# Performance work log

Measured on AMD Instinct MI355X. Metric: run time of the kernel, lower is better.

## Reference

```python
import jax, jax.numpy as jnp
import numpy as np

N_NODES = 100000
DROP_P = 0.1


def gcn_conv(x, W, b, row, col, n_nodes):
    """PyG GCNConv: out = D^{-1/2}(A+I)D^{-1/2} X W + b.
    row/col already include self-loops. Messages flow row(src) -> col(dst)."""
    xw = x @ W  # [N, H]
    deg = jax.ops.segment_sum(jnp.ones_like(col, dtype=xw.dtype), col, num_segments=n_nodes)
    dinv = jnp.where(deg > 0, jax.lax.rsqrt(deg), 0.0)
    norm = dinv[row] * dinv[col]  # [E]
    msg = norm[:, None] * xw[row]  # [E, H] gather + scale
    out = jax.ops.segment_sum(msg, col, num_segments=n_nodes)  # scatter-add
    return out + b


def dropout(x, key, p):
    keep = jax.random.bernoulli(key, 1.0 - p, x.shape)
    return jnp.where(keep, x / (1.0 - p), 0.0).astype(x.dtype)


def prelu(x, alpha):
    return jnp.where(x >= 0, x, alpha[None, :] * x)


def setup_inputs() -> dict:
    key = jax.random.key(0)
    k1, k2, k3, k4 = jax.random.split(key, 4)
    in_ch, hid = 128, 128
    n_edges = 1600000
    x = jax.random.normal(k1, (N_NODES, in_ch), dtype=jnp.float32)
    edge_index = jax.random.randint(k2, (2, n_edges), 0, N_NODES, dtype=jnp.int64)
    s = 1.0 / np.sqrt(in_ch)
    W1 = jax.random.normal(k3, (in_ch, hid), dtype=jnp.float32) * s
    W2 = jax.random.normal(k4, (hid, hid), dtype=jnp.float32) * s
    b1 = jnp.zeros((hid,), dtype=jnp.float32)
    b2 = jnp.zeros((hid,), dtype=jnp.float32)
    alpha = jnp.full((hid,), 0.25, dtype=jnp.float32)
    return {"x": x, "edge_index": edge_index, "W1": W1, "b1": b1,
            "W2": W2, "b2": b2, "alpha": alpha}


def reference(x, edge_index, W1, b1, W2, b2, alpha):
    n = x.shape[0]
    # add self-loops once (PyG default add_self_loops=True)
    loop = jnp.arange(n, dtype=edge_index.dtype)
    row = jnp.concatenate([edge_index[0], loop])
    col = jnp.concatenate([edge_index[1], loop])

    dk1, dk2 = jax.random.split(jax.random.key(42))
    h = gcn_conv(x, W1, b1, row, col, n)
    h = dropout(h, dk1, DROP_P)
    h = prelu(h, alpha)
    h = gcn_conv(h, W2, b2, row, col, n)
    h = dropout(h, dk2, DROP_P)
    h = prelu(h, alpha)
    return h
```

## Files before the change

### kernel.cpp

```cpp
#include <hip/hip_runtime.h>
#include <stdint.h>
#include <string.h>

__host__ __device__ inline uint32_t rotl32(uint32_t x, int r) {
    return (x << r) | (x >> (32 - r));
}

__host__ __device__ inline void tf2x32(uint32_t k0, uint32_t k1,
                                       uint32_t x0, uint32_t x1,
                                       uint32_t& o0, uint32_t& o1) {
    uint32_t ks0 = k0, ks1 = k1, ks2 = k0 ^ k1 ^ 0x1BD11BDAu;
    x0 += ks0; x1 += ks1;
#define TF_R4(a,b,c,d) \
    x0 += x1; x1 = rotl32(x1,a); x1 ^= x0; \
    x0 += x1; x1 = rotl32(x1,b); x1 ^= x0; \
    x0 += x1; x1 = rotl32(x1,c); x1 ^= x0; \
    x0 += x1; x1 = rotl32(x1,d); x1 ^= x0;
    TF_R4(13,15,26,6)  x0 += ks1; x1 += ks2 + 1u;
    TF_R4(17,29,16,24) x0 += ks2; x1 += ks0 + 2u;
    TF_R4(13,15,26,6)  x0 += ks0; x1 += ks1 + 3u;
    TF_R4(17,29,16,24) x0 += ks1; x1 += ks2 + 4u;
    TF_R4(13,15,26,6)  x0 += ks2; x1 += ks0 + 5u;
#undef TF_R4
    o0 = x0; o1 = x1;
}

__device__ inline unsigned pk2h(float a, float b) {
    _Float16 ha = (_Float16)a, hb = (_Float16)b;
    unsigned short ua, ub;
    __builtin_memcpy(&ua, &ha, 2);
    __builtin_memcpy(&ub, &hb, 2);
    return (unsigned)ua | ((unsigned)ub << 16);
}
__device__ inline unsigned short h16bits(float a) {
    _Float16 h = (_Float16)a;
    unsigned short u; __builtin_memcpy(&u, &h, 2);
    return u;
}
__device__ inline float lo16(unsigned u) {
    unsigned short s = (unsigned short)(u & 0xffffu);
    _Float16 h; __builtin_memcpy(&h, &s, 2);
    return (float)h;
}
__device__ inline float hi16(unsigned u) {
    unsigned short s = (unsigned short)(u >> 16);
    _Float16 h; __builtin_memcpy(&h, &s, 2);
    return (float)h;
}

typedef float fx4 __attribute__((ext_vector_type(4)));
typedef unsigned ux4 __attribute__((ext_vector_type(4)));
typedef _Float16 h16x8 __attribute__((ext_vector_type(8)));
typedef _Float16 h16x2 __attribute__((ext_vector_type(2)));
typedef float f32x4 __attribute__((ext_vector_type(4)));

__device__ inline h16x2 as_h2(unsigned u) { h16x2 r; __builtin_memcpy(&r, &u, 4); return r; }

#define CSR_CAP 48
#define NBKT 256
#define PART_EPB 8192

__global__ __launch_bounds__(256) void k_part(
        const int* __restrict__ ei, long long* __restrict__ gbkt,
        unsigned* __restrict__ gbcnt, int E, int N, int bw, int bcap) {
    __shared__ unsigned hcnt[NBKT], hoff[NBKT], hrun[NBKT];
    int t = (int)threadIdx.x;
    int base = blockIdx.x * PART_EPB;
    hcnt[t] = 0; hrun[t] = 0;
    __syncthreads();
    for (int i = 0; i < PART_EPB / 256; ++i) {
        int e = base + i * 256 + t;
        if (e < E) {
            int c = __builtin_nontemporal_load(ei + (size_t)E + e);
            int r = __builtin_nontemporal_load(ei + e);
            if ((unsigned)c < (unsigned)N && (unsigned)r < (unsigned)N)
                atomicAdd(&hcnt[(unsigned)c / (unsigned)bw], 1u);
        }
    }
    __syncthreads();
    hoff[t] = atomicAdd(&gbcnt[t], hcnt[t]);
    __syncthreads();
    for (int i = 0; i < PART_EPB / 256; ++i) {
        int e = base + i * 256 + t;
        if (e < E) {
            int c = ei[(size_t)E + e];
            int r = ei[e];
            if ((unsigned)c < (unsigned)N && (unsigned)r < (unsigned)N) {
                unsigned sp = (unsigned)c / (unsigned)bw;
                unsigned rank = atomicAdd(&hrun[sp], 1u);
                unsigned gp = hoff[sp] + rank;
                if (gp < (unsigned)bcap)
                    gbkt[(size_t)sp * bcap + gp] =
                        (long long)(unsigned)r | ((long long)(unsigned)c << 32);
            }
        }
    }
}

__global__ __launch_bounds__(256) void k_work(
        const long long* __restrict__ gbkt, const unsigned* __restrict__ gbcnt,
        unsigned* __restrict__ cnt, unsigned* __restrict__ csr,
        unsigned long long* __restrict__ m1, unsigned long long* __restrict__ m2,
        const float* __restrict__ x, unsigned* __restrict__ xb,
        const float* __restrict__ w1, const float* __restrict__ w2,
        _Float16* __restrict__ wt1, _Float16* __restrict__ wt2,
        unsigned k1a, unsigned k1b, unsigned k2a, unsigned k2b,
        int N, int bw, int bcap, int total, int MB, int CB) {
    __shared__ unsigned lcnt[512];
    int b = blockIdx.x;
    int t = (int)threadIdx.x;
    if (b < NBKT) {
        int lo = b * bw;
        int hi = lo + bw; if (hi > N) hi = N;
        int w = hi - lo; if (w < 0) w = 0;
        lcnt[t] = 0; lcnt[t + 256] = 0;
        __syncthreads();
        unsigned ne = gbcnt[b];
        if (ne > (unsigned)bcap) ne = (unsigned)bcap;
        const long long* base = gbkt + (size_t)b * bcap;
        for (unsigned e = t; e < ne; e += 256) {
            long long v = __builtin_nontemporal_load(base + e);
            unsigned r = (unsigned)(v & 0xffffffffll);
            unsigned c = (unsigned)(v >> 32);
            unsigned slot = atomicAdd(&lcnt[c - (unsigned)lo], 1u);
            if (slot < (unsigned)CSR_CAP)
                csr[(size_t)c * CSR_CAP + slot] = r;
        }
        __syncthreads();
        for (int i = t; i < w; i += 256)
            cnt[lo + i] = lcnt[i];
        return;
    }
    b -= NBKT;
    if (b < MB) {
        int wv = (b * 256 + t) >> 6;
        int lane = t & 63;
        int TW = (2 * total) >> 6;
        int half = total >> 6;
        int w0 = wv * 8;
#pragma unroll
        for (int j = 0; j < 8; j++) {
            int wd = w0 + j;
            if (wd < TW) {
                int wl = wd;
                unsigned ka = k1a, kb = k1b;
                unsigned long long* m = m1;
                if (wl >= half) { wl -= half; ka = k2a; kb = k2b; m = m2; }
                uint32_t o0, o1;
                tf2x32(ka, kb, 0u, (uint32_t)(wl * 64 + lane), o0, o1);
                bool keep = (((o0 ^ o1) >> 9) < 7549747u);
                unsigned long long bal = __ballot(keep);
                if (lane == 0)
                    __builtin_nontemporal_store(bal, m + wl);
            }
        }
        return;
    }
    b -= MB;
    if (b < CB) {
        int i = b * 256 + t;
        if (i < (total >> 3)) {
            const fx4* src = (const fx4*)(x + (size_t)i * 8);
            fx4 a = __builtin_nontemporal_load(src);
            fx4 bb = __builtin_nontemporal_load(src + 1);
            ux4 v;
            v.x = pk2h(a.x, a.y);
            v.y = pk2h(a.z, a.w);
            v.z = pk2h(bb.x, bb.y);
            v.w = pk2h(bb.z, bb.w);
            __builtin_nontemporal_store(v, (ux4*)xb + i);
        }
        return;
    }
    b -= CB;
    int idx = b * 256 + t;
    int mat = idx >> 14;
    int e2 = idx & 16383;
    int c = e2 >> 7, k = e2 & 127;
    const float* W = mat ? w2 : w1;
    _Float16* WT = mat ? wt2 : wt1;
    WT[(size_t)c * 128 + k] = (_Float16)W[(size_t)k * 128 + c];
}

__global__ __launch_bounds__(256) void k_prep(const unsigned* __restrict__ cnt,
        float* __restrict__ dinv, uint4* __restrict__ xb4, int N) {
    int i = blockIdx.x * 256 + (int)threadIdx.x;
    int node = i >> 4, part = i & 15;
    if (node >= N) return;
    float d = rsqrtf((float)cnt[node] + 1.0f);
    if (part == 0) dinv[node] = d;
    uint4 u = xb4[(size_t)node * 16 + part];
    uint4 o;
    o.x = pk2h(d * lo16(u.x), d * hi16(u.x));
    o.y = pk2h(d * lo16(u.y), d * hi16(u.y));
    o.z = pk2h(d * lo16(u.z), d * hi16(u.z));
    o.w = pk2h(d * lo16(u.w), d * hi16(u.w));
    xb4[(size_t)node * 16 + part] = o;
}

template <int OUT_HALF>
__global__ __launch_bounds__(128, 8) void k_layer(
        const unsigned short* __restrict__ in,
        const _Float16* __restrict__ WT,
        const float* __restrict__ bias, const float* __restrict__ alpha,
        const unsigned long long* __restrict__ mask,
        const float* __restrict__ dinv, const unsigned* __restrict__ cnt,
        const unsigned* __restrict__ csr,
        void* outv, int n) {
    __shared__ unsigned hls[32 * 68];
    int t = (int)threadIdx.x;
    int wv = t >> 6;
    int l = t & 63;
    int rowbase = blockIdx.x * 32 + wv * 16;
    unsigned* hl = hls + wv * 16 * 68;
    int slot = l >> 4;
    int lm = l & 15;
    int ci = lm << 3;

    int prow = rowbase + lm;
    bool pv = prow < n;
    float dnAll = pv ? dinv[prow] : 0.f;
    unsigned cAll = pv ? cnt[prow] : 0u;
    if (cAll > (unsigned)CSR_CAP) cAll = (unsigned)CSR_CAP;

#pragma unroll
    for (int g = 0; g < 4; ++g) {
        int rloc = g * 4 + slot;
        int node = rowbase + rloc;
        float dn = __shfl(dnAll, rloc);
        unsigned ecnt = (unsigned)__shfl((int)cAll, rloc);
        h16x2 a0 = (h16x2)0, a1 = (h16x2)0, a2 = (h16x2)0, a3 = (h16x2)0;
        size_t eb = (size_t)node * CSR_CAP;
        unsigned e = 0;
        unsigned nb4 = ecnt >> 2;
#pragma unroll 2
        for (unsigned bb = 0; bb < nb4; ++bb) {
            ux4 rr = __builtin_nontemporal_load((const ux4*)(csr + eb + e));
            uint4 u0 = *(const uint4*)(in + ((size_t)rr.x << 7) + ci);
            uint4 u1 = *(const uint4*)(in + ((size_t)rr.y << 7) + ci);
            uint4 u2 = *(const uint4*)(in + ((size_t)rr.z << 7) + ci);
            uint4 u3 = *(const uint4*)(in + ((size_t)rr.w << 7) + ci);
            a0 += as_h2(u0.x); a1 += as_h2(u0.y); a2 += as_h2(u0.z); a3 += as_h2(u0.w);
            a0 += as_h2(u1.x); a1 += as_h2(u1.y); a2 += as_h2(u1.z); a3 += as_h2(u1.w);
            a0 += as_h2(u2.x); a1 += as_h2(u2.y); a2 += as_h2(u2.z); a3 += as_h2(u2.w);
            a0 += as_h2(u3.x); a1 += as_h2(u3.y); a2 += as_h2(u3.z); a3 += as_h2(u3.w);
            e += 4;
        }
        for (; e < ecnt; ++e) {
            unsigned r0 = csr[eb + e];
            uint4 u0 = *(const uint4*)(in + ((size_t)r0 << 7) + ci);
            a0 += as_h2(u0.x); a1 += as_h2(u0.y); a2 += as_h2(u0.z); a3 += as_h2(u0.w);
        }
        if (node < n) {
            uint4 sv = *(const uint4*)(in + ((size_t)node << 7) + ci);
            a0 += as_h2(sv.x); a1 += as_h2(sv.y); a2 += as_h2(sv.z); a3 += as_h2(sv.w);
        }
        uint4 o;
        o.x = pk2h(dn * (float)a0[0], dn * (float)a0[1]);
        o.y = pk2h(dn * (float)a1[0], dn * (float)a1[1]);
        o.z = pk2h(dn * (float)a2[0], dn * (float)a2[1]);
        o.w = pk2h(dn * (float)a3[0], dn * (float)a3[1]);
        *(uint4*)(hl + (size_t)rloc * 68 + lm * 4) = o;
    }

    int kq = l >> 4;
    h16x8 afr[4];
#pragma unroll
    for (int kk = 0; kk < 4; kk++)
        afr[kk] = *(const h16x8*)(hl + (size_t)lm * 68 + kq * 4 + kk * 16);
#pragma unroll
    for (int f = 0; f < 8; f++) {
        f32x4 acc = (f32x4){0.f, 0.f, 0.f, 0.f};
#pragma unroll
        for (int kk = 0; kk < 4; kk++) {
            h16x8 bfr = *(const h16x8*)(WT + (size_t)(f * 16 + lm) * 128 + kk * 32 + kq * 8);
            acc = __builtin_amdgcn_mfma_f32_16x16x32_f16(afr[kk], bfr, acc, 0, 0, 0);
        }
        int c = f * 16 + lm;
        float bs = bias[c];
        float al = alpha[c];
#pragma unroll
        for (int j = 0; j < 4; j++) {
            int rl = kq * 4 + j;
            int rg = rowbase + rl;
            if (rg < n) {
                unsigned long long wmw = mask[((size_t)rg << 1) + (f >> 2)];
                bool keep = (wmw >> (c & 63)) & 1ull;
                float v = acc[j] + bs;
                v = keep ? v * (1.0f / 0.9f) : 0.0f;
                v = (v >= 0.f) ? v : al * v;
                if (OUT_HALF) {
                    float dnrow = __shfl(dnAll, rl);
                    __builtin_nontemporal_store(h16bits(v * dnrow),
                        (unsigned short*)outv + (size_t)rg * 128 + c);
                } else {
                    __builtin_nontemporal_store(v,
                        (float*)outv + (size_t)rg * 128 + c);
                }
            }
        }
    }
}

extern "C" void kernel_launch(void* const* d_in, const int* in_sizes, int n_in,
                              void* d_out, int out_size, void* d_ws, size_t ws_size,
                              hipStream_t stream) {
    const float* x  = (const float*)d_in[0];
    const int*   ei = (const int*)d_in[1];
    const float* W1 = (const float*)d_in[2];
    const float* b1 = (const float*)d_in[3];
    const float* W2 = (const float*)d_in[4];
    const float* b2 = (const float*)d_in[5];
    const float* al = (const float*)d_in[6];
    int N = in_sizes[0] / 128;
    int E = in_sizes[1] / 2;
    float* out = (float*)d_out;

    int bw = (N + NBKT - 1) / NBKT;
    int bcap = E / NBKT + E / NBKT / 4 + 1024;

    char* p = (char*)d_ws;
    unsigned short* xb = (unsigned short*)p;   p += (size_t)N * 128 * 2;
    unsigned short* ab = (unsigned short*)p;   p += (size_t)N * 128 * 2;
    long long* gbkt = (long long*)ab;
    unsigned* cnt = (unsigned*)p;              p += (size_t)N * 4;
    float* dinv = (float*)p;                   p += (size_t)N * 4;
    unsigned* csr = (unsigned*)p;              p += (size_t)N * CSR_CAP * 4;
    unsigned long long* m1 = (unsigned long long*)p;  p += ((size_t)N * 128 / 64) * 8;
    unsigned long long* m2 = (unsigned long long*)p;  p += ((size_t)N * 128 / 64) * 8;
    _Float16* wt1 = (_Float16*)p;              p += 128 * 128 * 2;
    _Float16* wt2 = (_Float16*)p;              p += 128 * 128 * 2;
    unsigned* gbcnt = (unsigned*)p;

    hipMemsetAsync(gbcnt, 0, NBKT * 4, stream);

    uint32_t dk1a, dk1b, dk2a, dk2b;
    tf2x32(0u, 42u, 0u, 0u, dk1a, dk1b);
    tf2x32(0u, 42u, 0u, 1u, dk2a, dk2b);

    int total = N * 128;
    int P1A = (E + PART_EPB - 1) / PART_EPB;
    k_part<<<P1A, 256, 0, stream>>>(ei, gbkt, gbcnt, E, N, bw, bcap);

    int TW = (2 * total) / 64;
    int MB = (TW + 31) / 32;
    int CB = (total / 8 + 255) / 256;
    int WB = (2 * 128 * 128 + 255) / 256;
    k_work<<<NBKT + MB + CB + WB, 256, 0, stream>>>(gbkt, gbcnt, cnt, csr,
                                                    m1, m2, x, (unsigned*)xb,
                                                    W1, W2, wt1, wt2,
                                                    dk1a, dk1b, dk2a, dk2b,
                                                    N, bw, bcap, total, MB, CB);
    k_prep<<<(N * 16 + 255) / 256, 256, 0, stream>>>(cnt, dinv, (uint4*)xb, N);

    int LB = (N + 31) / 32;
    k_layer<1><<<LB, 128, 0, stream>>>(xb, wt1, b1, al, m1, dinv, cnt, csr, ab, N);
    k_layer<0><<<LB, 128, 0, stream>>>(ab, wt2, b2, al, m2, dinv, cnt, csr, out, N);
}
```

Measured before the change: 322.2 us.

## Regroup preprocessing kernels: merge partition with mask/convert, fuse CSR build with scaling

The edge partition pass now runs in the same launch as dropout-mask generation, x conversion and weight transpose. The CSR-bucket build is fused with the dinv computation and the degree scaling of x, so the separate k_prep launch goes away. This cuts one kernel launch and lets the independent partition and elementwise work overlap. In exchange, the CSR/scale kernel now runs on only 256 blocks, so the scaling pass has less parallelism per node range.

```diff
diff --git a/kernel.cpp b/kernel.cpp
--- a/kernel.cpp
+++ b/kernel.cpp
@@ -62,76 +62,51 @@
 
 __global__ __launch_bounds__(256) void k_part(
         const int* __restrict__ ei, long long* __restrict__ gbkt,
-        unsigned* __restrict__ gbcnt, int E, int N, int bw, int bcap) {
-    __shared__ unsigned hcnt[NBKT], hoff[NBKT], hrun[NBKT];
-    int t = (int)threadIdx.x;
-    int base = blockIdx.x * PART_EPB;
-    hcnt[t] = 0; hrun[t] = 0;
-    __syncthreads();
-    for (int i = 0; i < PART_EPB / 256; ++i) {
-        int e = base + i * 256 + t;
-        if (e < E) {
-            int c = __builtin_nontemporal_load(ei + (size_t)E + e);
-            int r = __builtin_nontemporal_load(ei + e);
-            if ((unsigned)c < (unsigned)N && (unsigned)r < (unsigned)N)
-                atomicAdd(&hcnt[(unsigned)c / (unsigned)bw], 1u);
-        }
-    }
-    __syncthreads();
-    hoff[t] = atomicAdd(&gbcnt[t], hcnt[t]);
-    __syncthreads();
-    for (int i = 0; i < PART_EPB / 256; ++i) {
-        int e = base + i * 256 + t;
-        if (e < E) {
-            int c = ei[(size_t)E + e];
-            int r = ei[e];
-            if ((unsigned)c < (unsigned)N && (unsigned)r < (unsigned)N) {
-                unsigned sp = (unsigned)c / (unsigned)bw;
-                unsigned rank = atomicAdd(&hrun[sp], 1u);
-                unsigned gp = hoff[sp] + rank;
-                if (gp < (unsigned)bcap)
-                    gbkt[(size_t)sp * bcap + gp] =
-                        (long long)(unsigned)r | ((long long)(unsigned)c << 32);
-            }
-        }
-    }
-}
-
-__global__ __launch_bounds__(256) void k_work(
-        const long long* __restrict__ gbkt, const unsigned* __restrict__ gbcnt,
-        unsigned* __restrict__ cnt, unsigned* __restrict__ csr,
+        unsigned* __restrict__ gbcnt,
         unsigned long long* __restrict__ m1, unsigned long long* __restrict__ m2,
         const float* __restrict__ x, unsigned* __restrict__ xb,
         const float* __restrict__ w1, const float* __restrict__ w2,
         _Float16* __restrict__ wt1, _Float16* __restrict__ wt2,
         unsigned k1a, unsigned k1b, unsigned k2a, unsigned k2b,
-        int N, int bw, int bcap, int total, int MB, int CB) {
-    __shared__ unsigned lcnt[512];
+        int E, int N, int bw, int bcap, int total,
+        int PB, int MB, int CB) {
+    __shared__ unsigned hcnt[NBKT], hoff[NBKT], hrun[NBKT];
     int b = blockIdx.x;
     int t = (int)threadIdx.x;
-    if (b < NBKT) {
-        int lo = b * bw;
-        int hi = lo + bw; if (hi > N) hi = N;
-        int w = hi - lo; if (w < 0) w = 0;
-        lcnt[t] = 0; lcnt[t + 256] = 0;
+    if (b < PB) {
+        int base = b * PART_EPB;
+        hcnt[t] = 0; hrun[t] = 0;
         __syncthreads();
-        unsigned ne = gbcnt[b];
-        if (ne > (unsigned)bcap) ne = (unsigned)bcap;
-        const long long* base = gbkt + (size_t)b * bcap;
-        for (unsigned e = t; e < ne; e += 256) {
-            long long v = __builtin_nontemporal_load(base + e);
-            unsigned r = (unsigned)(v & 0xffffffffll);
-            unsigned c = (unsigned)(v >> 32);
-            unsigned slot = atomicAdd(&lcnt[c - (unsigned)lo], 1u);
-            if (slot < (unsigned)CSR_CAP)
-                csr[(size_t)c * CSR_CAP + slot] = r;
+        for (int i = 0; i < PART_EPB / 256; ++i) {
+            int e = base + i * 256 + t;
+            if (e < E) {
+                int c = __builtin_nontemporal_load(ei + (size_t)E + e);
+                int r = __builtin_nontemporal_load(ei + e);
+                if ((unsigned)c < (unsigned)N && (unsigned)r < (unsigned)N)
+                    atomicAdd(&hcnt[(unsigned)c / (unsigned)bw], 1u);
+            }
         }
         __syncthreads();
-        for (int i = t; i < w; i += 256)
-            cnt[lo + i] = lcnt[i];
+        hoff[t] = atomicAdd(&gbcnt[t], hcnt[t]);
+        __syncthreads();
+        for (int i = 0; i < PART_EPB / 256; ++i) {
+            int e = base + i * 256 + t;
+            if (e < E) {
+                int c = ei[(size_t)E + e];
+                int r = ei[e];
+                if ((unsigned)c < (unsigned)N && (unsigned)r < (unsigned)N) {
+                    unsigned sp = (unsigned)c / (unsigned)bw;
+                    unsigned rank = atomicAdd(&hrun[sp], 1u);
+                    unsigned gp = hoff[sp] + rank;
+                    if (gp < (unsigned)bcap)
+                        gbkt[(size_t)sp * bcap + gp] =
+                            (long long)(unsigned)r | ((long long)(unsigned)c << 32);
+                }
+            }
+        }
         return;
     }
-    b -= NBKT;
+    b -= PB;
     if (b < MB) {
         int wv = (b * 256 + t) >> 6;
         int lane = t & 63;
@@ -182,20 +157,46 @@
     WT[(size_t)c * 128 + k] = (_Float16)W[(size_t)k * 128 + c];
 }
 
-__global__ __launch_bounds__(256) void k_prep(const unsigned* __restrict__ cnt,
-        float* __restrict__ dinv, uint4* __restrict__ xb4, int N) {
-    int i = blockIdx.x * 256 + (int)threadIdx.x;
-    int node = i >> 4, part = i & 15;
-    if (node >= N) return;
-    float d = rsqrtf((float)cnt[node] + 1.0f);
-    if (part == 0) dinv[node] = d;
-    uint4 u = xb4[(size_t)node * 16 + part];
-    uint4 o;
-    o.x = pk2h(d * lo16(u.x), d * hi16(u.x));
-    o.y = pk2h(d * lo16(u.y), d * hi16(u.y));
-    o.z = pk2h(d * lo16(u.z), d * hi16(u.z));
-    o.w = pk2h(d * lo16(u.w), d * hi16(u.w));
-    xb4[(size_t)node * 16 + part] = o;
+__global__ __launch_bounds__(256) void k_work(
+        const long long* __restrict__ gbkt, const unsigned* __restrict__ gbcnt,
+        unsigned* __restrict__ cnt, unsigned* __restrict__ csr,
+        float* __restrict__ dinv, uint4* __restrict__ xb4,
+        int N, int bw, int bcap) {
+    __shared__ unsigned lcnt[512];
+    int b = blockIdx.x;
+    int t = (int)threadIdx.x;
+    int lo = b * bw;
+    int hi = lo + bw; if (hi > N) hi = N;
+    int w = hi - lo; if (w < 0) w = 0;
+    lcnt[t] = 0; lcnt[t + 256] = 0;
+    __syncthreads();
+    unsigned ne = gbcnt[b];
+    if (ne > (unsigned)bcap) ne = (unsigned)bcap;
+    const long long* base = gbkt + (size_t)b * bcap;
+    for (unsigned e = t; e < ne; e += 256) {
+        long long v = __builtin_nontemporal_load(base + e);
+        unsigned r = (unsigned)(v & 0xffffffffll);
+        unsigned c = (unsigned)(v >> 32);
+        unsigned slot = atomicAdd(&lcnt[c - (unsigned)lo], 1u);
+        if (slot < (unsigned)CSR_CAP)
+            csr[(size_t)c * CSR_CAP + slot] = r;
+    }
+    __syncthreads();
+    for (int i = t; i < w; i += 256)
+        cnt[lo + i] = lcnt[i];
+    for (int idx = t; idx < w * 16; idx += 256) {
+        int nl = idx >> 4, part = idx & 15;
+        int node = lo + nl;
+        float d = rsqrtf((float)lcnt[nl] + 1.0f);
+        if (part == 0) dinv[node] = d;
+        uint4 u = xb4[(size_t)node * 16 + part];
+        uint4 o;
+        o.x = pk2h(d * lo16(u.x), d * hi16(u.x));
+        o.y = pk2h(d * lo16(u.y), d * hi16(u.y));
+        o.z = pk2h(d * lo16(u.z), d * hi16(u.z));
+        o.w = pk2h(d * lo16(u.w), d * hi16(u.w));
+        xb4[(size_t)node * 16 + part] = o;
+    }
 }
 
 template <int OUT_HALF>
@@ -339,19 +340,19 @@
     tf2x32(0u, 42u, 0u, 1u, dk2a, dk2b);
 
     int total = N * 128;
-    int P1A = (E + PART_EPB - 1) / PART_EPB;
-    k_part<<<P1A, 256, 0, stream>>>(ei, gbkt, gbcnt, E, N, bw, bcap);
-
+    int PB = (E + PART_EPB - 1) / PART_EPB;
     int TW = (2 * total) / 64;
     int MB = (TW + 31) / 32;
     int CB = (total / 8 + 255) / 256;
     int WB = (2 * 128 * 128 + 255) / 256;
-    k_work<<<NBKT + MB + CB + WB, 256, 0, stream>>>(gbkt, gbcnt, cnt, csr,
-                                                    m1, m2, x, (unsigned*)xb,
-                                                    W1, W2, wt1, wt2,
-                                                    dk1a, dk1b, dk2a, dk2b,
-                                                    N, bw, bcap, total, MB, CB);
-    k_prep<<<(N * 16 + 255) / 256, 256, 0, stream>>>(cnt, dinv, (uint4*)xb, N);
+    k_part<<<PB + MB + CB + WB, 256, 0, stream>>>(ei, gbkt, gbcnt, m1, m2,
+                                                  x, (unsigned*)xb,
+                                                  W1, W2, wt1, wt2,
+                                                  dk1a, dk1b, dk2a, dk2b,
+                                                  E, N, bw, bcap, total,
+                                                  PB, MB, CB);
+    k_work<<<NBKT, 256, 0, stream>>>(gbkt, gbcnt, cnt, csr, dinv, (uint4*)xb,
+                                     N, bw, bcap);
 
     int LB = (N + 31) / 32;
     k_layer<1><<<LB, 128, 0, stream>>>(xb, wt1, b1, al, m1, dinv, cnt, csr, ab, N);
```

Result: faster. 299.4 us, median of 2 (-7.1%).
